# Performance work log

Measured on AMD Instinct MI355X. Metric: run time of the kernel, lower is better.

## Reference

```python
import jax, jax.numpy as jnp
import numpy as np

NUM_NODES = 50000
NUM_HYPEREDGES = 50000
NNZ = 800000
IN_CH, HID_CH, OUT_CH = 512, 256, 64


def setup_inputs() -> dict:
    key = jax.random.key(0)
    k = jax.random.split(key, 6)
    x = jax.random.normal(k[0], (NUM_NODES, IN_CH), dtype=jnp.float32)
    node_idx = jax.random.randint(k[1], (NNZ,), 0, NUM_NODES)
    hedge_idx = jax.random.randint(k[2], (NNZ,), 0, NUM_HYPEREDGES)
    edge_index = jnp.stack([node_idx, hedge_idx]).astype(jnp.int64)
    W1 = jax.random.normal(k[3], (IN_CH, HID_CH), dtype=jnp.float32) * (1.0 / np.sqrt(IN_CH))
    b1 = jnp.zeros((HID_CH,), dtype=jnp.float32)
    W2 = jax.random.normal(k[4], (HID_CH, OUT_CH), dtype=jnp.float32) * (1.0 / np.sqrt(HID_CH))
    b2 = jnp.zeros((OUT_CH,), dtype=jnp.float32)
    return {"x": x, "edge_index": edge_index, "W1": W1, "b1": b1, "W2": W2, "b2": b2}


def hypergraph_conv(x, node_idx, hedge_idx, W, b):
    # x' = D^{-1} H B^{-1} H^T (x Theta) + b   (PyG HypergraphConv, unit edge weights)
    h = x @ W                                   # [N, F_out]
    ones = jnp.ones(node_idx.shape[0], dtype=x.dtype)
    D = jax.ops.segment_sum(ones, node_idx, num_segments=NUM_NODES)        # node degree
    B = jax.ops.segment_sum(ones, hedge_idx, num_segments=NUM_HYPEREDGES)  # hyperedge degree
    D_inv = jnp.where(D > 0, 1.0 / D, 0.0)
    B_inv = jnp.where(B > 0, 1.0 / B, 0.0)
    # node -> hyperedge aggregation
    m = jax.ops.segment_sum(h[node_idx], hedge_idx, num_segments=NUM_HYPEREDGES)
    m = m * B_inv[:, None]                      # [E, F_out]
    # hyperedge -> node aggregation
    out = jax.ops.segment_sum(m[hedge_idx], node_idx, num_segments=NUM_NODES)
    out = out * D_inv[:, None]                  # [N, F_out]
    return out + b


def reference(x, edge_index, W1, b1, W2, b2):
    node_idx = edge_index[0]
    hedge_idx = edge_index[1]
    h = hypergraph_conv(x, node_idx, hedge_idx, W1, b1)
    h = jax.nn.relu(h)
    h = hypergraph_conv(h, node_idx, hedge_idx, W2, b2)
    return jax.nn.log_softmax(h, axis=1)
```

## Files before the change

kernel.cpp:

```cpp
#include <hip/hip_runtime.h>
#include <math.h>

#define N_NODES  50000
#define N_HEDGES 50000
#define NNZ_     800000
#define IN_CH    512
#define HID_CH   256
#define OUT_CH   64
#define M_PAD    50048
#define NBK      391

#define CVT_BLK  25000
#define BH_BLK   98
#define PK1_BLK  512
#define PK2_BLK  64

typedef __attribute__((ext_vector_type(8))) short bf16x8;
typedef __attribute__((ext_vector_type(4))) float f32x4;

__device__ __forceinline__ unsigned short f2bf(float f) {
    union { float f; unsigned u; } v; v.f = f;
    unsigned r = v.u + 0x7FFFu + ((v.u >> 16) & 1u);
    return (unsigned short)(r >> 16);
}
__device__ __forceinline__ float bf2f(unsigned short u) {
    union { unsigned u; float f; } v; v.u = (unsigned)u << 16; return v.f;
}

#define GLL16(g, l)                                                            \
    __builtin_amdgcn_global_load_lds(                                          \
        (const __attribute__((address_space(1))) void*)(g),                    \
        (__attribute__((address_space(3))) void*)(l), 16, 0, 0)

__global__ void prep_kernel(const float* __restrict__ x, unsigned short* __restrict__ x_bf,
                            const float* __restrict__ W1, unsigned short* __restrict__ Wp1,
                            const float* __restrict__ W2, unsigned short* __restrict__ Wp2,
                            const int* __restrict__ ni, const int* __restrict__ hi,
                            int* __restrict__ bcntN, int* __restrict__ bcntH) {
    const int blk = blockIdx.x;
    const int t = threadIdx.x;
    if (blk < CVT_BLK) {
        const long i = (long)blk * 256 + t;
        const float4 v = *(const float4*)(x + i * 4);
        ushort4 o;
        o.x = f2bf(v.x); o.y = f2bf(v.y); o.z = f2bf(v.z); o.w = f2bf(v.w);
        *(ushort4*)(x_bf + i * 4) = o;
    } else if (blk < CVT_BLK + BH_BLK) {
        __shared__ int lh[NBK], ln[NBK];
        for (int k = t; k < NBK; k += 256) { lh[k] = 0; ln[k] = 0; }
        __syncthreads();
        const int bb = blk - CVT_BLK;
        for (int i4 = bb * 256 + t; i4 < NNZ_ / 4; i4 += BH_BLK * 256) {
            const int4 nv = *(const int4*)(ni + i4 * 4);
            const int4 hv = *(const int4*)(hi + i4 * 4);
            atomicAdd(&ln[nv.x >> 7], 1); atomicAdd(&ln[nv.y >> 7], 1);
            atomicAdd(&ln[nv.z >> 7], 1); atomicAdd(&ln[nv.w >> 7], 1);
            atomicAdd(&lh[hv.x >> 7], 1); atomicAdd(&lh[hv.y >> 7], 1);
            atomicAdd(&lh[hv.z >> 7], 1); atomicAdd(&lh[hv.w >> 7], 1);
        }
        __syncthreads();
        for (int k = t; k < NBK; k += 256) {
            if (ln[k]) atomicAdd(&bcntN[k], ln[k]);
            if (lh[k]) atomicAdd(&bcntH[k], lh[k]);
        }
    } else if (blk < CVT_BLK + BH_BLK + PK1_BLK) {
        const int i = (blk - (CVT_BLK + BH_BLK)) * 256 + t;
        const int kt = i / (HID_CH * 32);
        const int r  = i % (HID_CH * 32);
        const int n  = r >> 5, kk = r & 31;
        Wp1[i] = f2bf(W1[(size_t)(kt * 32 + kk) * HID_CH + n]);
    } else {
        const int i = (blk - (CVT_BLK + BH_BLK + PK1_BLK)) * 256 + t;
        const int kt = i / (OUT_CH * 32);
        const int r  = i % (OUT_CH * 32);
        const int n  = r >> 5, kk = r & 31;
        Wp2[i] = f2bf(W2[(size_t)(kt * 32 + kk) * OUT_CH + n]);
    }
}

__global__ void scan391_kernel(const int* __restrict__ cA, int* __restrict__ offA,
                               int* __restrict__ curA,
                               const int* __restrict__ cB, int* __restrict__ offB,
                               int* __restrict__ curB) {
    const int* cnt = blockIdx.x ? cB : cA;
    int* off = blockIdx.x ? offB : offA;
    int* cur = blockIdx.x ? curB : curA;
    __shared__ int sbuf[512];
    const int t = threadIdx.x;
    const int v = (t < NBK) ? cnt[t] : 0;
    sbuf[t] = v;
    __syncthreads();
    #pragma unroll
    for (int d = 1; d < 512; d <<= 1) {
        int u = (t >= d) ? sbuf[t - d] : 0;
        __syncthreads();
        sbuf[t] += u;
        __syncthreads();
    }
    if (t < NBK) { off[t] = sbuf[t] - v; cur[t] = sbuf[t] - v; }
    if (t == NBK - 1) off[NBK] = sbuf[t];
}

__global__ void bin_kernel(const int* __restrict__ ni, const int* __restrict__ hi,
                           int* __restrict__ bcurN, int* __restrict__ bcurH,
                           unsigned* __restrict__ recN, unsigned* __restrict__ recH) {
    __shared__ int cH[NBK], cN[NBK], bH[NBK], bN[NBK];
    for (int t = threadIdx.x; t < NBK; t += blockDim.x) { cH[t] = 0; cN[t] = 0; }
    __syncthreads();
    const int gid = blockIdx.x * blockDim.x + threadIdx.x;
    const int i0 = gid * 4;
    int4 nv, hv;
    const bool act = (i0 < NNZ_);
    if (act) {
        nv = *(const int4*)(ni + i0);
        hv = *(const int4*)(hi + i0);
        atomicAdd(&cN[nv.x >> 7], 1); atomicAdd(&cN[nv.y >> 7], 1);
        atomicAdd(&cN[nv.z >> 7], 1); atomicAdd(&cN[nv.w >> 7], 1);
        atomicAdd(&cH[hv.x >> 7], 1); atomicAdd(&cH[hv.y >> 7], 1);
        atomicAdd(&cH[hv.z >> 7], 1); atomicAdd(&cH[hv.w >> 7], 1);
    }
    __syncthreads();
    for (int t = threadIdx.x; t < NBK; t += blockDim.x) {
        bH[t] = cH[t] ? atomicAdd(&bcurH[t], cH[t]) : 0;
        bN[t] = cN[t] ? atomicAdd(&bcurN[t], cN[t]) : 0;
    }
    __syncthreads();
    for (int t = threadIdx.x; t < NBK; t += blockDim.x) { cH[t] = bH[t]; cN[t] = bN[t]; }
    __syncthreads();
    if (act) {
        int nn[4] = {nv.x, nv.y, nv.z, nv.w};
        int hh[4] = {hv.x, hv.y, hv.z, hv.w};
        #pragma unroll
        for (int k = 0; k < 4; ++k) {
            int p = atomicAdd(&cH[hh[k] >> 7], 1);
            recH[p] = ((unsigned)(hh[k] & 127) << 16) | (unsigned)nn[k];
            p = atomicAdd(&cN[nn[k] >> 7], 1);
            recN[p] = ((unsigned)(nn[k] & 127) << 16) | (unsigned)hh[k];
        }
    }
}

__global__ void buildcsr_kernel(const int* __restrict__ bstartH, const unsigned* __restrict__ recH,
                                int* __restrict__ offH, int* __restrict__ colH,
                                float* __restrict__ Binv,
                                const int* __restrict__ bstartN, const unsigned* __restrict__ recN,
                                int* __restrict__ offN, int* __restrict__ colN,
                                float* __restrict__ Dinv) {
    int b = blockIdx.x;
    const int* bstart; const unsigned* rec; int* off; int* col; float* inv;
    if (b < NBK) { bstart = bstartH; rec = recH; off = offH; col = colH; inv = Binv; }
    else { b -= NBK; bstart = bstartN; rec = recN; off = offN; col = colN; inv = Dinv; }
    const int s = bstart[b], e = bstart[b + 1];
    const int t = threadIdx.x;
    __shared__ int lc[128], ps[128], cur[128];
    if (t < 128) lc[t] = 0;
    __syncthreads();
    for (int i = s + t; i < e; i += 256) atomicAdd(&lc[rec[i] >> 16], 1);
    __syncthreads();
    if (t < 128) ps[t] = lc[t];
    __syncthreads();
    #pragma unroll
    for (int d = 1; d < 128; d <<= 1) {
        int v = (t >= d && t < 128) ? ps[t - d] : 0;
        __syncthreads();
        if (t < 128) ps[t] += v;
        __syncthreads();
    }
    if (t < 128) {
        const int excl = s + ps[t] - lc[t];
        cur[t] = excl;
        const int id = b * 128 + t;
        if (id < N_NODES) {
            off[id] = excl;
            inv[id] = lc[t] > 0 ? 1.f / (float)lc[t] : 0.f;
        }
    }
    if (b == NBK - 1 && t == 255) off[N_NODES] = bstart[NBK];
    __syncthreads();
    for (int i = s + t; i < e; i += 256) {
        const unsigned r = rec[i];
        const int p = atomicAdd(&cur[r >> 16], 1);
        col[p] = (int)(r & 0xFFFFu);
    }
}

template <int BN>
__global__ void mfma_gemm_kernel(const unsigned short* __restrict__ A,
                                 const unsigned short* __restrict__ Wp,
                                 unsigned short* __restrict__ C, int M, int N, int K) {
    constexpr int NT = BN / 32;
    __shared__ unsigned short As[128 * 32];
    __shared__ unsigned short Bs[BN * 32];

    const int tid  = threadIdx.x;
    const int wave = tid >> 6;
    const int lane = tid & 63;
    const int wr = wave >> 1;
    const int wc = wave & 1;
    const int quad = lane >> 4;
    const int l15  = lane & 15;
    const int row0 = blockIdx.y * 128;
    const int col0 = blockIdx.x * BN;

    const size_t a_g0   = (size_t)(row0 + wave * 16 + (lane >> 2)) * K + (lane & 3) * 8;
    const int    a_l0   = (wave * 16 + (lane >> 2)) * 32 + (lane & 3) * 8;
    const size_t b_gbase = ((size_t)col0 + wave * 16 + (lane >> 2)) * 32 + (lane & 3) * 8;
    const int    b_l0   = (wave * 16 + (lane >> 2)) * 32 + (lane & 3) * 8;

    f32x4 acc[4][NT];
    #pragma unroll
    for (int mt = 0; mt < 4; ++mt)
        #pragma unroll
        for (int nt = 0; nt < NT; ++nt)
            acc[mt][nt] = (f32x4)0.f;

    const int KT = K / 32;
    for (int kt = 0; kt < KT; ++kt) {
        __syncthreads();
        GLL16(A + a_g0 + (size_t)kt * 32, As + a_l0);
        GLL16(A + a_g0 + (size_t)(kt * 32) + (size_t)64 * K, As + a_l0 + 64 * 32);
        const size_t bk = (size_t)kt * N * 32;
        GLL16(Wp + bk + b_gbase, Bs + b_l0);
        if (BN == 128)
            GLL16(Wp + bk + b_gbase + 64 * 32, Bs + b_l0 + 64 * 32);
        __syncthreads();

        bf16x8 af[4], bf[NT];
        #pragma unroll
        for (int mt = 0; mt < 4; ++mt)
            af[mt] = *(const bf16x8*)(As + (wr * 64 + mt * 16 + l15) * 32 + quad * 8);
        #pragma unroll
        for (int nt = 0; nt < NT; ++nt)
            bf[nt] = *(const bf16x8*)(Bs + (wc * (BN / 2) + nt * 16 + l15) * 32 + quad * 8);
        #pragma unroll
        for (int mt = 0; mt < 4; ++mt)
            #pragma unroll
            for (int nt = 0; nt < NT; ++nt)
                acc[mt][nt] = __builtin_amdgcn_mfma_f32_16x16x32_bf16(
                    af[mt], bf[nt], acc[mt][nt], 0, 0, 0);
    }

    #pragma unroll
    for (int mt = 0; mt < 4; ++mt) {
        const int gr0 = row0 + wr * 64 + mt * 16 + quad * 4;
        #pragma unroll
        for (int nt = 0; nt < NT; ++nt) {
            const int gc = col0 + wc * (BN / 2) + nt * 16 + l15;
            #pragma unroll
            for (int r = 0; r < 4; ++r) {
                int gr = gr0 + r;
                if (gr < M) C[(size_t)gr * N + gc] = f2bf(acc[mt][nt][r]);
            }
        }
    }
}

template <bool EPI>
__global__ void gather256_kernel(const unsigned short* __restrict__ src,
                                 unsigned short* __restrict__ dst,
                                 const int* __restrict__ off, const int* __restrict__ col,
                                 const float* __restrict__ scale,
                                 const float* __restrict__ bias, int nrows) {
    int row = blockIdx.x * (blockDim.x >> 6) + (threadIdx.x >> 6);
    if (row >= nrows) return;
    int lane = threadIdx.x & 63;
    int s = off[row], e = off[row + 1];
    float ax = 0.f, ay = 0.f, az = 0.f, aw = 0.f;
    int j = s;
    for (; j + 3 < e; j += 4) {
        const ushort4 u0 = *(const ushort4*)(src + (size_t)col[j]     * HID_CH + (lane << 2));
        const ushort4 u1 = *(const ushort4*)(src + (size_t)col[j + 1] * HID_CH + (lane << 2));
        const ushort4 u2 = *(const ushort4*)(src + (size_t)col[j + 2] * HID_CH + (lane << 2));
        const ushort4 u3 = *(const ushort4*)(src + (size_t)col[j + 3] * HID_CH + (lane << 2));
        ax += (bf2f(u0.x) + bf2f(u1.x)) + (bf2f(u2.x) + bf2f(u3.x));
        ay += (bf2f(u0.y) + bf2f(u1.y)) + (bf2f(u2.y) + bf2f(u3.y));
        az += (bf2f(u0.z) + bf2f(u1.z)) + (bf2f(u2.z) + bf2f(u3.z));
        aw += (bf2f(u0.w) + bf2f(u1.w)) + (bf2f(u2.w) + bf2f(u3.w));
    }
    for (; j < e; ++j) {
        const ushort4 u = *(const ushort4*)(src + (size_t)col[j] * HID_CH + (lane << 2));
        ax += bf2f(u.x); ay += bf2f(u.y); az += bf2f(u.z); aw += bf2f(u.w);
    }
    float sc = scale[row];
    float rx = ax * sc, ry = ay * sc, rz = az * sc, rw = aw * sc;
    if (EPI) {
        const float4 b = *(const float4*)(bias + (lane << 2));
        rx = fmaxf(rx + b.x, 0.f); ry = fmaxf(ry + b.y, 0.f);
        rz = fmaxf(rz + b.z, 0.f); rw = fmaxf(rw + b.w, 0.f);
    }
    ushort4 o;
    o.x = f2bf(rx); o.y = f2bf(ry); o.z = f2bf(rz); o.w = f2bf(rw);
    *(ushort4*)(dst + (size_t)row * HID_CH + (lane << 2)) = o;
}

template <bool LSM>
__global__ void gather64_kernel(const unsigned short* __restrict__ src, void* __restrict__ dstv,
                                const int* __restrict__ off, const int* __restrict__ col,
                                const float* __restrict__ scale,
                                const float* __restrict__ bias, int nrows) {
    int row = blockIdx.x * (blockDim.x >> 6) + (threadIdx.x >> 6);
    if (row >= nrows) return;
    const int lane = threadIdx.x & 63;
    const int g = lane >> 4;
    const int l = lane & 15;
    const int s = off[row], e = off[row + 1];
    float a0 = 0.f, a1 = 0.f, a2 = 0.f, a3 = 0.f;
    int j = s + g;
    for (; j + 4 < e; j += 8) {
        const ushort4 u0 = *(const ushort4*)(src + ((size_t)col[j]     << 6) + (l << 2));
        const ushort4 u1 = *(const ushort4*)(src + ((size_t)col[j + 4] << 6) + (l << 2));
        a0 += bf2f(u0.x) + bf2f(u1.x); a1 += bf2f(u0.y) + bf2f(u1.y);
        a2 += bf2f(u0.z) + bf2f(u1.z); a3 += bf2f(u0.w) + bf2f(u1.w);
    }
    if (j < e) {
        const ushort4 u = *(const ushort4*)(src + ((size_t)col[j] << 6) + (l << 2));
        a0 += bf2f(u.x); a1 += bf2f(u.y); a2 += bf2f(u.z); a3 += bf2f(u.w);
    }
    a0 += __shfl_xor(a0, 16); a1 += __shfl_xor(a1, 16);
    a2 += __shfl_xor(a2, 16); a3 += __shfl_xor(a3, 16);
    a0 += __shfl_xor(a0, 32); a1 += __shfl_xor(a1, 32);
    a2 += __shfl_xor(a2, 32); a3 += __shfl_xor(a3, 32);
    const float sc = scale[row];
    float v0 = a0 * sc, v1 = a1 * sc, v2 = a2 * sc, v3 = a3 * sc;
    if (LSM) {
        const float4 b = *(const float4*)(bias + (l << 2));
        v0 += b.x; v1 += b.y; v2 += b.z; v3 += b.w;
        float m = fmaxf(fmaxf(v0, v1), fmaxf(v2, v3));
        #pragma unroll
        for (int o = 8; o >= 1; o >>= 1) m = fmaxf(m, __shfl_xor(m, o));
        float su = expf(v0 - m) + expf(v1 - m) + expf(v2 - m) + expf(v3 - m);
        #pragma unroll
        for (int o = 8; o >= 1; o >>= 1) su += __shfl_xor(su, o);
        const float lg = m + logf(su);
        if (g == 0) {
            float4 o4;
            o4.x = v0 - lg; o4.y = v1 - lg; o4.z = v2 - lg; o4.w = v3 - lg;
            *(float4*)((float*)dstv + (size_t)row * OUT_CH + (l << 2)) = o4;
        }
    } else if (g == 0) {
        ushort4 o4;
        o4.x = f2bf(v0); o4.y = f2bf(v1); o4.z = f2bf(v2); o4.w = f2bf(v3);
        *(ushort4*)((unsigned short*)dstv + (size_t)row * OUT_CH + (l << 2)) = o4;
    }
}

extern "C" void kernel_launch(void* const* d_in, const int* in_sizes, int n_in,
                              void* d_out, int out_size, void* d_ws, size_t ws_size,
                              hipStream_t stream) {
    const float* x  = (const float*)d_in[0];
    const int*   ei = (const int*)d_in[1];
    const float* W1 = (const float*)d_in[2];
    const float* b1 = (const float*)d_in[3];
    const float* W2 = (const float*)d_in[4];
    const float* b2 = (const float*)d_in[5];
    float* out = (float*)d_out;

    const int* node_idx  = ei;
    const int* hedge_idx = ei + NNZ_;

    const size_t RCAP = (size_t)M_PAD * IN_CH / 2;
    float* regionA = (float*)d_ws;
    float* regionB = regionA + RCAP;
    float* Dinv = regionB + RCAP;
    float* Binv = Dinv + N_NODES;
    int* offN = (int*)(Binv + N_HEDGES);
    int* offH = offN + N_NODES + 1;
    int* colN = offH + N_HEDGES + 1;
    int* colH = colN + NNZ_;
    unsigned short* Wp1 = (unsigned short*)(colH + NNZ_);
    unsigned short* Wp2 = Wp1 + IN_CH * HID_CH;
    int* bcntH   = (int*)(Wp2 + HID_CH * OUT_CH);
    int* bcntN   = bcntH + 400;
    int* bstartH = bcntN + 400;
    int* bstartN = bstartH + 400;
    int* bcurH   = bstartN + 400;
    int* bcurN   = bcurH + 400;

    unsigned* recH = (unsigned*)regionA;
    unsigned* recN = recH + NNZ_;

    unsigned short* x_bf  = (unsigned short*)regionB;
    unsigned short* h1_bf = (unsigned short*)regionA;
    unsigned short* m1_bf = (unsigned short*)regionB;
    unsigned short* h2_bf = (unsigned short*)regionA;
    unsigned short* g_bf  = (unsigned short*)regionB;
    unsigned short* m2_bf = (unsigned short*)regionB + (size_t)M_PAD * OUT_CH;

    hipMemsetAsync(bcntH, 0, 800 * sizeof(int), stream);
    prep_kernel<<<CVT_BLK + BH_BLK + PK1_BLK + PK2_BLK, 256, 0, stream>>>(
        x, x_bf, W1, Wp1, W2, Wp2, node_idx, hedge_idx, bcntN, bcntH);
    scan391_kernel<<<2, 512, 0, stream>>>(bcntH, bstartH, bcurH, bcntN, bstartN, bcurN);
    bin_kernel<<<200, 1024, 0, stream>>>(node_idx, hedge_idx, bcurN, bcurH, recN, recH);
    buildcsr_kernel<<<2 * NBK, 256, 0, stream>>>(bstartH, recH, offH, colH, Binv,
                                                 bstartN, recN, offN, colN, Dinv);

    mfma_gemm_kernel<128><<<dim3(HID_CH / 128, (N_NODES + 127) / 128), 256, 0, stream>>>(
        x_bf, Wp1, h1_bf, N_NODES, HID_CH, IN_CH);
    gather256_kernel<false><<<(N_HEDGES + 3) / 4, 256, 0, stream>>>(
        h1_bf, m1_bf, offH, colH, Binv, nullptr, N_HEDGES);
    gather256_kernel<true><<<(N_NODES + 3) / 4, 256, 0, stream>>>(
        m1_bf, h2_bf, offN, colN, Dinv, b1, N_NODES);

    mfma_gemm_kernel<64><<<dim3(OUT_CH / 64, (N_NODES + 127) / 128), 256, 0, stream>>>(
        h2_bf, Wp2, g_bf, N_NODES, OUT_CH, HID_CH);
    gather64_kernel<false><<<(N_HEDGES + 3) / 4, 256, 0, stream>>>(
        g_bf, m2_bf, offH, colH, Binv, nullptr, N_HEDGES);
    gather64_kernel<true><<<(N_NODES + 3) / 4, 256, 0, stream>>>(
        m2_bf, out, offN, colN, Dinv, b2, N_NODES);
}
```

Baseline: 420.4 us.

## Fuse fp32-to-bf16 conversion of x into first GEMM and widen 256-wide gathers

```diff
diff --git a/kernel.cpp b/kernel.cpp
--- a/kernel.cpp
+++ b/kernel.cpp
@@ -10,7 +10,6 @@
 #define M_PAD    50048
 #define NBK      391
 
-#define CVT_BLK  25000
 #define BH_BLK   98
 #define PK1_BLK  512
 #define PK2_BLK  64
@@ -32,25 +31,17 @@
         (const __attribute__((address_space(1))) void*)(g),                    \
         (__attribute__((address_space(3))) void*)(l), 16, 0, 0)
 
-__global__ void prep_kernel(const float* __restrict__ x, unsigned short* __restrict__ x_bf,
-                            const float* __restrict__ W1, unsigned short* __restrict__ Wp1,
+__global__ void prep_kernel(const float* __restrict__ W1, unsigned short* __restrict__ Wp1,
                             const float* __restrict__ W2, unsigned short* __restrict__ Wp2,
                             const int* __restrict__ ni, const int* __restrict__ hi,
                             int* __restrict__ bcntN, int* __restrict__ bcntH) {
     const int blk = blockIdx.x;
     const int t = threadIdx.x;
-    if (blk < CVT_BLK) {
-        const long i = (long)blk * 256 + t;
-        const float4 v = *(const float4*)(x + i * 4);
-        ushort4 o;
-        o.x = f2bf(v.x); o.y = f2bf(v.y); o.z = f2bf(v.z); o.w = f2bf(v.w);
-        *(ushort4*)(x_bf + i * 4) = o;
-    } else if (blk < CVT_BLK + BH_BLK) {
+    if (blk < BH_BLK) {
         __shared__ int lh[NBK], ln[NBK];
         for (int k = t; k < NBK; k += 256) { lh[k] = 0; ln[k] = 0; }
         __syncthreads();
-        const int bb = blk - CVT_BLK;
-        for (int i4 = bb * 256 + t; i4 < NNZ_ / 4; i4 += BH_BLK * 256) {
+        for (int i4 = blk * 256 + t; i4 < NNZ_ / 4; i4 += BH_BLK * 256) {
             const int4 nv = *(const int4*)(ni + i4 * 4);
             const int4 hv = *(const int4*)(hi + i4 * 4);
             atomicAdd(&ln[nv.x >> 7], 1); atomicAdd(&ln[nv.y >> 7], 1);
@@ -63,14 +54,14 @@
             if (ln[k]) atomicAdd(&bcntN[k], ln[k]);
             if (lh[k]) atomicAdd(&bcntH[k], lh[k]);
         }
-    } else if (blk < CVT_BLK + BH_BLK + PK1_BLK) {
-        const int i = (blk - (CVT_BLK + BH_BLK)) * 256 + t;
+    } else if (blk < BH_BLK + PK1_BLK) {
+        const int i = (blk - BH_BLK) * 256 + t;
         const int kt = i / (HID_CH * 32);
         const int r  = i % (HID_CH * 32);
         const int n  = r >> 5, kk = r & 31;
         Wp1[i] = f2bf(W1[(size_t)(kt * 32 + kk) * HID_CH + n]);
     } else {
-        const int i = (blk - (CVT_BLK + BH_BLK + PK1_BLK)) * 256 + t;
+        const int i = (blk - (BH_BLK + PK1_BLK)) * 256 + t;
         const int kt = i / (OUT_CH * 32);
         const int r  = i % (OUT_CH * 32);
         const int n  = r >> 5, kk = r & 31;
@@ -184,6 +175,92 @@
     }
 }
 
+__global__ void gemm1_fused_kernel(const float* __restrict__ X,
+                                   const unsigned short* __restrict__ Wp,
+                                   unsigned short* __restrict__ C, int M) {
+    constexpr int BM = 64, BN = 256, K = IN_CH, KT = K / 32;
+    __shared__ unsigned short As[BM * 32];
+    __shared__ unsigned short Bs[BN * 32];
+    const int tid  = threadIdx.x;
+    const int wave = tid >> 6;
+    const int lane = tid & 63;
+    const int wr = wave >> 1;
+    const int wc = wave & 1;
+    const int quad = lane >> 4;
+    const int l15  = lane & 15;
+    const int row0 = blockIdx.x * BM;
+
+    float4 va[2];
+    auto loadA = [&](int kt) {
+        #pragma unroll
+        for (int r = 0; r < 2; ++r) {
+            const int idx = r * 256 + tid;
+            const int row = idx >> 3;
+            const int kc  = (idx & 7) * 4;
+            const int gr  = row0 + row;
+            float4 v = make_float4(0.f, 0.f, 0.f, 0.f);
+            if (gr < M) v = *(const float4*)(X + (size_t)gr * K + kt * 32 + kc);
+            va[r] = v;
+        }
+    };
+
+    f32x4 acc[2][8];
+    #pragma unroll
+    for (int mt = 0; mt < 2; ++mt)
+        #pragma unroll
+        for (int nt = 0; nt < 8; ++nt)
+            acc[mt][nt] = (f32x4)0.f;
+
+    loadA(0);
+    for (int kt = 0; kt < KT; ++kt) {
+        __syncthreads();
+        #pragma unroll
+        for (int r = 0; r < 2; ++r) {
+            const int idx = r * 256 + tid;
+            const int row = idx >> 3;
+            const int kc  = (idx & 7) * 4;
+            ushort4 o;
+            o.x = f2bf(va[r].x); o.y = f2bf(va[r].y);
+            o.z = f2bf(va[r].z); o.w = f2bf(va[r].w);
+            *(ushort4*)(As + row * 32 + kc) = o;
+        }
+        const size_t bk = (size_t)kt * BN * 32;
+        #pragma unroll
+        for (int r = 0; r < 4; ++r)
+            GLL16(Wp + bk + r * 2048 + (size_t)tid * 8, Bs + r * 2048 + tid * 8);
+        __syncthreads();
+        if (kt + 1 < KT) loadA(kt + 1);
+
+        bf16x8 af[2], bfr[8];
+        #pragma unroll
+        for (int mt = 0; mt < 2; ++mt)
+            af[mt] = *(const bf16x8*)(As + (wr * 32 + mt * 16 + l15) * 32 + quad * 8);
+        #pragma unroll
+        for (int nt = 0; nt < 8; ++nt)
+            bfr[nt] = *(const bf16x8*)(Bs + (wc * 128 + nt * 16 + l15) * 32 + quad * 8);
+        #pragma unroll
+        for (int mt = 0; mt < 2; ++mt)
+            #pragma unroll
+            for (int nt = 0; nt < 8; ++nt)
+                acc[mt][nt] = __builtin_amdgcn_mfma_f32_16x16x32_bf16(
+                    af[mt], bfr[nt], acc[mt][nt], 0, 0, 0);
+    }
+
+    #pragma unroll
+    for (int mt = 0; mt < 2; ++mt) {
+        const int gr0 = row0 + wr * 32 + mt * 16 + quad * 4;
+        #pragma unroll
+        for (int nt = 0; nt < 8; ++nt) {
+            const int gc = wc * 128 + nt * 16 + l15;
+            #pragma unroll
+            for (int r = 0; r < 4; ++r) {
+                const int gr = gr0 + r;
+                if (gr < M) C[(size_t)gr * HID_CH + gc] = f2bf(acc[mt][nt][r]);
+            }
+        }
+    }
+}
+
 template <int BN>
 __global__ void mfma_gemm_kernel(const unsigned short* __restrict__ A,
                                  const unsigned short* __restrict__ Wp,
@@ -263,34 +340,45 @@
                                  const float* __restrict__ bias, int nrows) {
     int row = blockIdx.x * (blockDim.x >> 6) + (threadIdx.x >> 6);
     if (row >= nrows) return;
-    int lane = threadIdx.x & 63;
-    int s = off[row], e = off[row + 1];
-    float ax = 0.f, ay = 0.f, az = 0.f, aw = 0.f;
-    int j = s;
-    for (; j + 3 < e; j += 4) {
-        const ushort4 u0 = *(const ushort4*)(src + (size_t)col[j]     * HID_CH + (lane << 2));
-        const ushort4 u1 = *(const ushort4*)(src + (size_t)col[j + 1] * HID_CH + (lane << 2));
-        const ushort4 u2 = *(const ushort4*)(src + (size_t)col[j + 2] * HID_CH + (lane << 2));
-        const ushort4 u3 = *(const ushort4*)(src + (size_t)col[j + 3] * HID_CH + (lane << 2));
-        ax += (bf2f(u0.x) + bf2f(u1.x)) + (bf2f(u2.x) + bf2f(u3.x));
-        ay += (bf2f(u0.y) + bf2f(u1.y)) + (bf2f(u2.y) + bf2f(u3.y));
-        az += (bf2f(u0.z) + bf2f(u1.z)) + (bf2f(u2.z) + bf2f(u3.z));
-        aw += (bf2f(u0.w) + bf2f(u1.w)) + (bf2f(u2.w) + bf2f(u3.w));
-    }
-    for (; j < e; ++j) {
-        const ushort4 u = *(const ushort4*)(src + (size_t)col[j] * HID_CH + (lane << 2));
-        ax += bf2f(u.x); ay += bf2f(u.y); az += bf2f(u.z); aw += bf2f(u.w);
-    }
-    float sc = scale[row];
-    float rx = ax * sc, ry = ay * sc, rz = az * sc, rw = aw * sc;
+    const int lane = threadIdx.x & 63;
+    const int g = lane >> 5;
+    const int l = lane & 31;
+    const int s = off[row], e = off[row + 1];
+    float a[8];
+    #pragma unroll
+    for (int k = 0; k < 8; ++k) a[k] = 0.f;
+    int j = s + g;
+    for (; j + 2 < e; j += 4) {
+        const bf16x8 u0 = *(const bf16x8*)(src + ((size_t)col[j]     << 8) + (l << 3));
+        const bf16x8 u1 = *(const bf16x8*)(src + ((size_t)col[j + 2] << 8) + (l << 3));
+        #pragma unroll
+        for (int k = 0; k < 8; ++k)
+            a[k] += bf2f((unsigned short)u0[k]) + bf2f((unsigned short)u1[k]);
+    }
+    if (j < e) {
+        const bf16x8 u = *(const bf16x8*)(src + ((size_t)col[j] << 8) + (l << 3));
+        #pragma unroll
+        for (int k = 0; k < 8; ++k) a[k] += bf2f((unsigned short)u[k]);
+    }
+    #pragma unroll
+    for (int k = 0; k < 8; ++k) a[k] += __shfl_xor(a[k], 32);
+    if (g != 0) return;
+    const float sc = scale[row];
+    float v[8];
+    #pragma unroll
+    for (int k = 0; k < 8; ++k) v[k] = a[k] * sc;
     if (EPI) {
-        const float4 b = *(const float4*)(bias + (lane << 2));
-        rx = fmaxf(rx + b.x, 0.f); ry = fmaxf(ry + b.y, 0.f);
-        rz = fmaxf(rz + b.z, 0.f); rw = fmaxf(rw + b.w, 0.f);
-    }
-    ushort4 o;
-    o.x = f2bf(rx); o.y = f2bf(ry); o.z = f2bf(rz); o.w = f2bf(rw);
-    *(ushort4*)(dst + (size_t)row * HID_CH + (lane << 2)) = o;
+        const float4 b0 = *(const float4*)(bias + (l << 3));
+        const float4 b1 = *(const float4*)(bias + (l << 3) + 4);
+        v[0] = fmaxf(v[0] + b0.x, 0.f); v[1] = fmaxf(v[1] + b0.y, 0.f);
+        v[2] = fmaxf(v[2] + b0.z, 0.f); v[3] = fmaxf(v[3] + b0.w, 0.f);
+        v[4] = fmaxf(v[4] + b1.x, 0.f); v[5] = fmaxf(v[5] + b1.y, 0.f);
+        v[6] = fmaxf(v[6] + b1.z, 0.f); v[7] = fmaxf(v[7] + b1.w, 0.f);
+    }
+    bf16x8 o;
+    #pragma unroll
+    for (int k = 0; k < 8; ++k) o[k] = (short)f2bf(v[k]);
+    *(bf16x8*)(dst + ((size_t)row << 8) + (l << 3)) = o;
 }
 
 template <bool LSM>
@@ -379,7 +467,6 @@
     unsigned* recH = (unsigned*)regionA;
     unsigned* recN = recH + NNZ_;
 
-    unsigned short* x_bf  = (unsigned short*)regionB;
     unsigned short* h1_bf = (unsigned short*)regionA;
     unsigned short* m1_bf = (unsigned short*)regionB;
     unsigned short* h2_bf = (unsigned short*)regionA;
@@ -387,15 +474,14 @@
     unsigned short* m2_bf = (unsigned short*)regionB + (size_t)M_PAD * OUT_CH;
 
     hipMemsetAsync(bcntH, 0, 800 * sizeof(int), stream);
-    prep_kernel<<<CVT_BLK + BH_BLK + PK1_BLK + PK2_BLK, 256, 0, stream>>>(
-        x, x_bf, W1, Wp1, W2, Wp2, node_idx, hedge_idx, bcntN, bcntH);
+    prep_kernel<<<BH_BLK + PK1_BLK + PK2_BLK, 256, 0, stream>>>(
+        W1, Wp1, W2, Wp2, node_idx, hedge_idx, bcntN, bcntH);
     scan391_kernel<<<2, 512, 0, stream>>>(bcntH, bstartH, bcurH, bcntN, bstartN, bcurN);
     bin_kernel<<<200, 1024, 0, stream>>>(node_idx, hedge_idx, bcurN, bcurH, recN, recH);
     buildcsr_kernel<<<2 * NBK, 256, 0, stream>>>(bstartH, recH, offH, colH, Binv,
                                                  bstartN, recN, offN, colN, Dinv);
 
-    mfma_gemm_kernel<128><<<dim3(HID_CH / 128, (N_NODES + 127) / 128), 256, 0, stream>>>(
-        x_bf, Wp1, h1_bf, N_NODES, HID_CH, IN_CH);
+    gemm1_fused_kernel<<<(N_NODES + 63) / 64, 256, 0, stream>>>(x, Wp1, h1_bf, N_NODES);
     gather256_kernel<false><<<(N_HEDGES + 3) / 4, 256, 0, stream>>>(
         h1_bf, m1_bf, offH, colH, Binv, nullptr, N_HEDGES);
     gather256_kernel<true><<<(N_NODES + 3) / 4, 256, 0, stream>>>(
```

After: 401.8 us. 1.05x faster.
